# Kernel optimization log

Hardware: AMD Instinct MI355X
Metric: run time of the kernel (lower is better)

## Reference

```python
import jax, jax.numpy as jnp
import numpy as np

MAX_SHIFT_BANDS = 2.0


def setup_inputs() -> dict:
    key = jax.random.key(0)
    k1, k2 = jax.random.split(key)
    B, Bh, H, W = 4, 128, 256, 256
    x = jax.random.normal(k1, (B, Bh, H, W), dtype=jnp.float32)
    wavelength_shift = jax.random.normal(k2, (B, Bh, W), dtype=jnp.float32)
    return {"x": x, "wavelength_shift": wavelength_shift}


def reference(x, wavelength_shift):
    # Faithful to torch grid_sample(mode='bilinear', padding_mode='border',
    # align_corners=False) applied along the spectral (band) axis only.
    B, Bh, H, W = x.shape
    dt = x.dtype

    shift = jnp.clip(wavelength_shift, -MAX_SHIFT_BANDS, MAX_SHIFT_BANDS)
    shift = shift[:, :, None, :]                         # [B,Bh,1,W]
    band = jnp.arange(Bh, dtype=dt)[None, :, None, None]  # [1,Bh,1,1]
    shifted = jnp.clip(band + shift, 0.0, Bh - 1)        # [B,Bh,1,W]

    # grid_sample align_corners=False unnormalization:
    # grid g = shifted/(Bh-1)*2 - 1 ; iy = ((g+1)*Bh - 1)/2 = shifted*Bh/(Bh-1) - 0.5
    iy = shifted * (Bh / (Bh - 1)) - 0.5                 # [B,Bh,1,W]
    i0f = jnp.floor(iy)
    w = iy - i0f                                          # lerp weight, [B,Bh,1,W]
    i0 = i0f.astype(jnp.int32)                            # may be -1 at low edge
    i0c = jnp.clip(i0, 0, Bh - 1)                         # border padding
    i1c = jnp.clip(i0 + 1, 0, Bh - 1)

    # broadcast gather indices over H rows
    i0c = jnp.broadcast_to(i0c, (B, Bh, H, W))
    i1c = jnp.broadcast_to(i1c, (B, Bh, H, W))

    x0 = jnp.take_along_axis(x, i0c, axis=1)              # [B,Bh,H,W]
    x1 = jnp.take_along_axis(x, i1c, axis=1)
    return x0 * (1.0 - w) + x1 * w
```

## Files before the change

### kernel.cpp

```cpp
#include <hip/hip_runtime.h>


#define BH_  128
#define H_   256
#define W_   256
#define TB    32
#define NLDS (TB + 6)

__global__ __launch_bounds__(512) void smile_kernel(
    const float* __restrict__ x,
    const float* __restrict__ ws,
    float* __restrict__ out)
{
    __shared__ float tile[NLDS + 1][W_];

    const int bid0 = blockIdx.x;
    const int bid  = (bid0 & 7) * 512 + (bid0 >> 3);

    const int tileI = bid & 3;
    const int rem   = bid >> 2;
    const int h   = rem & (H_ - 1);
    const int b   = rem >> 8;
    const int bh0 = tileI * TB;

    const int t    = threadIdx.x;
    const int wave = t >> 6;
    const int lane = t & 63;

    const float* __restrict__ xsrc = x + (size_t)b * (BH_ * H_ * W_) + h * W_;

#pragma unroll
    for (int j = 0; j < 3; ++j) {
        const int  i  = wave + j * 8;
        const bool rl = (i < 22);
        const int band = min(max(bh0 - 3 + (rl ? i : 0), 0), BH_ - 1);
        const float* gp = xsrc + (size_t)band * (H_ * W_) + lane * 4;
        __builtin_amdgcn_global_load_lds(
            (const __attribute__((address_space(1))) void*)gp,
            (__attribute__((address_space(3))) void*)&tile[rl ? i : NLDS][0],
            16, 0, 0);
    }
    __builtin_amdgcn_sched_barrier(0);

    const int bhbase = bh0 + wave * 4;
    const float* __restrict__ wsb = ws + (size_t)(b * BH_ + bhbase) * W_ + lane;
    float s[4][4];
#pragma unroll
    for (int r = 0; r < 4; ++r)
#pragma unroll
        for (int j = 0; j < 4; ++j)
            s[r][j] = wsb[r * W_ + j * 64];
    __builtin_amdgcn_sched_barrier(0);

#pragma unroll
    for (int j = 0; j < 2; ++j) {
        const int i = 22 + wave + j * 8;
        const int band = min(max(bh0 - 3 + i, 0), BH_ - 1);
        const float* gp = xsrc + (size_t)band * (H_ * W_) + lane * 4;
        __builtin_amdgcn_global_load_lds(
            (const __attribute__((address_space(1))) void*)gp,
            (__attribute__((address_space(3))) void*)&tile[i][0],
            16, 0, 0);
    }
    __builtin_amdgcn_sched_barrier(0);

    const float scale = (float)(128.0 / 127.0);
    float* __restrict__ outp =
        out + (((size_t)b * BH_ + bhbase) * H_ + h) * W_ + lane;

    auto COMPUTE = [&]() {
#pragma unroll
        for (int r = 0; r < 4; ++r) {
            const int bh = bhbase + r;
#pragma unroll
            for (int j = 0; j < 4; ++j) {
                const int w = lane + j * 64;
                float sc      = fminf(fmaxf(s[r][j], -2.0f), 2.0f);
                float shifted = fminf(fmaxf((float)bh + sc, 0.0f),
                                      (float)(BH_ - 1));
                float iy      = fmaf(shifted, scale, -0.5f);
                float i0f     = floorf(iy);
                float frac    = iy - i0f;
                int   i0      = (int)i0f;
                int   r0      = min(max(i0, 0), BH_ - 1) - bh0 + 3;
                int   r1      = min(i0 + 1, BH_ - 1) - bh0 + 3;
                float x0 = tile[r0][w];
                float x1 = tile[r1][w];
                __builtin_nontemporal_store(
                    fmaf(frac, x1 - x0, x0),
                    outp + (size_t)r * (H_ * W_) + j * 64);
            }
        }
    };

    asm volatile("s_waitcnt vmcnt(2)" ::: "memory");
    __builtin_amdgcn_s_barrier();
    asm volatile("" ::: "memory");

    if (wave < 4) {
        COMPUTE();
    }

    if (wave < 4) {
        asm volatile("s_waitcnt vmcnt(16)" ::: "memory");
    } else {
        asm volatile("s_waitcnt vmcnt(0)" ::: "memory");
    }
    __builtin_amdgcn_s_barrier();
    asm volatile("" ::: "memory");

    if (wave >= 4) {
        COMPUTE();
    }
}

extern "C" void kernel_launch(void* const* d_in, const int* in_sizes, int n_in,
                              void* d_out, int out_size, void* d_ws, size_t ws_size,
                              hipStream_t stream) {
    const float* x  = (const float*)d_in[0];
    const float* ws = (const float*)d_in[1];
    float* out = (float*)d_out;

    const int grid = 4 * H_ * (BH_ / TB);
    smile_kernel<<<grid, 512, 0, stream>>>(x, ws, out);
}
```

Baseline: 45.23 us.

## Interleave band-row staging with shift loads and compute in four pipelined groups

Each wave now handles bands strided by 8 (`bh0 + g*8 + wave`) instead of 4 contiguous bands. The LDS staging of band rows is interleaved with the per-group shift loads. Compute then proceeds in four stages, each gated by a progressively looser `s_waitcnt vmcnt` plus a barrier. All waves start producing output once the first rows arrive, instead of half the waves waiting for all loads. This adds more block barriers, and relies on hand-counted vmcnt thresholds that must stay consistent with the issued store and load counts.

```diff
diff --git a/kernel.cpp b/kernel.cpp
--- a/kernel.cpp
+++ b/kernel.cpp
@@ -29,89 +29,89 @@
 
     const float* __restrict__ xsrc = x + (size_t)b * (BH_ * H_ * W_) + h * W_;
 
-#pragma unroll
-    for (int j = 0; j < 3; ++j) {
-        const int  i  = wave + j * 8;
-        const bool rl = (i < 22);
+    auto STAGE_ROW = [&](int i) {
+        const bool rl = (i < NLDS);
         const int band = min(max(bh0 - 3 + (rl ? i : 0), 0), BH_ - 1);
         const float* gp = xsrc + (size_t)band * (H_ * W_) + lane * 4;
         __builtin_amdgcn_global_load_lds(
             (const __attribute__((address_space(1))) void*)gp,
             (__attribute__((address_space(3))) void*)&tile[rl ? i : NLDS][0],
             16, 0, 0);
-    }
+    };
+
+    const float* __restrict__ wsb =
+        ws + (size_t)(b * BH_ + bh0 + wave) * W_ + lane;
+    float s[4][4];
+
+    STAGE_ROW(wave);  STAGE_ROW(wave + 8);
     __builtin_amdgcn_sched_barrier(0);
-
-    const int bhbase = bh0 + wave * 4;
-    const float* __restrict__ wsb = ws + (size_t)(b * BH_ + bhbase) * W_ + lane;
-    float s[4][4];
 #pragma unroll
-    for (int r = 0; r < 4; ++r)
+    for (int j = 0; j < 4; ++j) s[0][j] = wsb[0 * 8 * W_ + j * 64];
+    __builtin_amdgcn_sched_barrier(0);
+    STAGE_ROW(wave + 16);
+    __builtin_amdgcn_sched_barrier(0);
 #pragma unroll
-        for (int j = 0; j < 4; ++j)
-            s[r][j] = wsb[r * W_ + j * 64];
+    for (int j = 0; j < 4; ++j) s[1][j] = wsb[1 * 8 * W_ + j * 64];
     __builtin_amdgcn_sched_barrier(0);
-
+    STAGE_ROW(wave + 24);
+    __builtin_amdgcn_sched_barrier(0);
 #pragma unroll
-    for (int j = 0; j < 2; ++j) {
-        const int i = 22 + wave + j * 8;
-        const int band = min(max(bh0 - 3 + i, 0), BH_ - 1);
-        const float* gp = xsrc + (size_t)band * (H_ * W_) + lane * 4;
-        __builtin_amdgcn_global_load_lds(
-            (const __attribute__((address_space(1))) void*)gp,
-            (__attribute__((address_space(3))) void*)&tile[i][0],
-            16, 0, 0);
-    }
+    for (int j = 0; j < 4; ++j) s[2][j] = wsb[2 * 8 * W_ + j * 64];
+    __builtin_amdgcn_sched_barrier(0);
+    STAGE_ROW(wave + 32);
+    __builtin_amdgcn_sched_barrier(0);
+#pragma unroll
+    for (int j = 0; j < 4; ++j) s[3][j] = wsb[3 * 8 * W_ + j * 64];
     __builtin_amdgcn_sched_barrier(0);
 
     const float scale = (float)(128.0 / 127.0);
-    float* __restrict__ outp =
-        out + (((size_t)b * BH_ + bhbase) * H_ + h) * W_ + lane;
+    float* __restrict__ outbase =
+        out + (((size_t)b * BH_ + bh0 + wave) * H_ + h) * W_ + lane;
 
-    auto COMPUTE = [&]() {
+    auto COMPUTE = [&](int g) {
+        const int bh = bh0 + g * 8 + wave;
+        float* __restrict__ outp = outbase + (size_t)(g * 8) * (H_ * W_);
 #pragma unroll
-        for (int r = 0; r < 4; ++r) {
-            const int bh = bhbase + r;
-#pragma unroll
-            for (int j = 0; j < 4; ++j) {
-                const int w = lane + j * 64;
-                float sc      = fminf(fmaxf(s[r][j], -2.0f), 2.0f);
-                float shifted = fminf(fmaxf((float)bh + sc, 0.0f),
-                                      (float)(BH_ - 1));
-                float iy      = fmaf(shifted, scale, -0.5f);
-                float i0f     = floorf(iy);
-                float frac    = iy - i0f;
-                int   i0      = (int)i0f;
-                int   r0      = min(max(i0, 0), BH_ - 1) - bh0 + 3;
-                int   r1      = min(i0 + 1, BH_ - 1) - bh0 + 3;
-                float x0 = tile[r0][w];
-                float x1 = tile[r1][w];
-                __builtin_nontemporal_store(
-                    fmaf(frac, x1 - x0, x0),
-                    outp + (size_t)r * (H_ * W_) + j * 64);
-            }
+        for (int j = 0; j < 4; ++j) {
+            const int w = lane + j * 64;
+            float sc      = fminf(fmaxf(s[g][j], -2.0f), 2.0f);
+            float shifted = fminf(fmaxf((float)bh + sc, 0.0f),
+                                  (float)(BH_ - 1));
+            float iy      = fmaf(shifted, scale, -0.5f);
+            float i0f     = floorf(iy);
+            float frac    = iy - i0f;
+            int   i0      = (int)i0f;
+            int   r0      = min(max(i0, 0), BH_ - 1) - bh0 + 3;
+            int   r1      = min(i0 + 1, BH_ - 1) - bh0 + 3;
+            float x0 = tile[r0][w];
+            float x1 = tile[r1][w];
+            __builtin_nontemporal_store(fmaf(frac, x1 - x0, x0),
+                                        outp + j * 64);
         }
     };
 
-    asm volatile("s_waitcnt vmcnt(2)" ::: "memory");
+    asm volatile("s_waitcnt vmcnt(15)" ::: "memory");
     __builtin_amdgcn_s_barrier();
-    asm volatile("" ::: "memory");
+    __builtin_amdgcn_sched_barrier(0);
+    COMPUTE(0);
+    __builtin_amdgcn_sched_barrier(0);
 
-    if (wave < 4) {
-        COMPUTE();
-    }
+    asm volatile("s_waitcnt vmcnt(14)" ::: "memory");
+    __builtin_amdgcn_s_barrier();
+    __builtin_amdgcn_sched_barrier(0);
+    COMPUTE(1);
+    __builtin_amdgcn_sched_barrier(0);
 
-    if (wave < 4) {
-        asm volatile("s_waitcnt vmcnt(16)" ::: "memory");
-    } else {
-        asm volatile("s_waitcnt vmcnt(0)" ::: "memory");
-    }
+    asm volatile("s_waitcnt vmcnt(13)" ::: "memory");
     __builtin_amdgcn_s_barrier();
-    asm volatile("" ::: "memory");
+    __builtin_amdgcn_sched_barrier(0);
+    COMPUTE(2);
+    __builtin_amdgcn_sched_barrier(0);
 
-    if (wave >= 4) {
-        COMPUTE();
-    }
+    asm volatile("s_waitcnt vmcnt(12)" ::: "memory");
+    __builtin_amdgcn_s_barrier();
+    __builtin_amdgcn_sched_barrier(0);
+    COMPUTE(3);
 }
 
 extern "C" void kernel_launch(void* const* d_in, const int* in_sizes, int n_in,
```

After: 45.28 us. No clear change (+0.1%).
